# Optimization experiments

Measured on AMD Instinct MI355X. Metric: run time of the kernel, lower is better.

## Reference

```python
import jax, jax.numpy as jnp
import numpy as np

B, N = 2, 6
C_IN, C_MID = 512, 512
D, C_OUT = 112, 80
OGH, OGW, DS = 256, 704, 16
FH, FW = OGH // DS, OGW // DS  # 16, 44
D_MIN, D_MAX = 2.0, 58.0
NX, NY, NZ = 128, 128, 1
VSIZE = np.array([0.8, 0.8, 8.0], dtype=np.float32)
VCOORD = np.array([-51.2 + 0.4, -51.2 + 0.4, -5.0 + 4.0], dtype=np.float32)


def make_frustum():
    # (D, FH, FW, 4) with entries (x_pix, y_pix, depth, 1)
    ones = jnp.ones((D, FH, FW), jnp.float32)
    d = jnp.linspace(D_MIN, D_MAX, D)[:, None, None] * jnp.ones((1, FH, FW))
    x = jnp.linspace(0.0, OGW - 1.0, FW)[None, None, :] * jnp.ones((D, FH, 1))
    y = jnp.linspace(0.0, OGH - 1.0, FH)[None, :, None] * jnp.ones((D, 1, FW))
    return jnp.stack([x, y, d, ones], axis=-1)


def setup_inputs() -> dict:
    key = jax.random.key(0)
    ks = jax.random.split(key, 24)
    eye = jnp.eye(4, dtype=jnp.float32)
    K = jnp.array([[1266.0, 0.0, 800.0, 0.0],
                   [0.0, 1266.0, 450.0, 0.0],
                   [0.0, 0.0, 1.0, 0.0],
                   [0.0, 0.0, 0.0, 1.0]], jnp.float32)
    inp = {
        'feat': jax.random.normal(ks[0], (B * N, C_IN, FH, FW), jnp.float32),
        'w1': 0.05 * jax.random.normal(ks[1], (C_MID, C_IN, 3, 3), jnp.float32),
        'g1': 1.0 + 0.1 * jax.random.normal(ks[2], (C_MID,), jnp.float32),
        'b1': 0.1 * jax.random.normal(ks[3], (C_MID,), jnp.float32),
        'm1': 0.1 * jax.random.normal(ks[4], (C_MID,), jnp.float32),
        'v1': 0.5 + jax.random.uniform(ks[5], (C_MID,), jnp.float32),
        'w2': 0.05 * jax.random.normal(ks[6], (C_MID, C_MID, 3, 3), jnp.float32),
        'g2': 1.0 + 0.1 * jax.random.normal(ks[7], (C_MID,), jnp.float32),
        'b2': 0.1 * jax.random.normal(ks[8], (C_MID,), jnp.float32),
        'm2': 0.1 * jax.random.normal(ks[9], (C_MID,), jnp.float32),
        'v2': 0.5 + jax.random.uniform(ks[10], (C_MID,), jnp.float32),
        'w_out': 0.05 * jax.random.normal(ks[11], (D + C_OUT, C_MID, 1, 1), jnp.float32),
        'b_out': 0.1 * jax.random.normal(ks[12], (D + C_OUT,), jnp.float32),
        'sensor2ego': eye + 0.05 * jax.random.normal(ks[13], (B, N, 4, 4), jnp.float32),
        'sensor2virtual': eye + 0.05 * jax.random.normal(ks[14], (B, N, 4, 4), jnp.float32),
        'intrin': K + 0.01 * jax.random.normal(ks[15], (B, N, 4, 4), jnp.float32),
        'ida': eye + 0.01 * jax.random.normal(ks[16], (B, N, 4, 4), jnp.float32),
        'ref_heights': 1.5 + 0.2 * jax.random.normal(ks[17], (B, N), jnp.float32),
        'bda': eye + 0.01 * jax.random.normal(ks[18], (B, 4, 4), jnp.float32),
    }
    return inp


def _conv(x, w, p):
    return jax.lax.conv_general_dilated(x, w, (1, 1), [(p, p), (p, p)],
                                         dimension_numbers=('NCHW', 'OIHW', 'NCHW'))


def _bn(x, g, b, m, v):
    s = (g / jnp.sqrt(v + 1e-5))
    return (x - m[None, :, None, None]) * s[None, :, None, None] + b[None, :, None, None]


def get_geometry(sensor2ego, sensor2virtual, intrin, ida, ref_heights, bda):
    frustum = make_frustum()[..., None]  # (D,FH,FW,4,1)
    pts = jnp.linalg.inv(ida)[:, :, None, None, None] @ frustum  # (B,N,D,FH,FW,4,1)
    ref = ref_heights[:, :, None, None, None, None]
    height = -pts[..., 2, :] + ref  # (B,N,D,FH,FW,1)
    pc = pts.at[..., 2, :].set(10.0)
    pc = jnp.concatenate([pc[..., :2, :] * pc[..., 2:3, :], pc[..., 2:, :]], axis=-2)
    cv = sensor2virtual @ jnp.linalg.inv(intrin)
    pv = cv[:, :, None, None, None] @ pc
    ratio = height[..., 0] / pv[..., 1, 0]  # (B,N,D,FH,FW)
    pts = pv * ratio[..., None, None]
    pts = pts.at[..., 3, :].set(1.0)
    ce = sensor2ego @ jnp.linalg.inv(sensor2virtual)
    pts = ce[:, :, None, None, None] @ pts
    pts = (bda[:, None, None, None, None] @ pts)[..., 0]
    return pts[..., :3]  # (B,N,D,FH,FW,3)


def reference(feat, w1, g1, b1, m1, v1, w2, g2, b2, m2, v2, w_out, b_out,
              sensor2ego, sensor2virtual, intrin, ida, ref_heights, bda):
    # DepthNet head
    h = jax.nn.relu(_bn(_conv(feat, w1, 1), g1, b1, m1, v1))
    h = jax.nn.relu(_bn(_conv(h, w2, 1), g2, b2, m2, v2))
    hf = _conv(h, w_out, 0) + b_out[None, :, None, None]  # (B*N, D+C, FH, FW)
    depth = jax.nn.softmax(hf[:, :D], axis=1).reshape(B, N, D, FH, FW)
    context = hf[:, D:].reshape(B, N, C_OUT, FH, FW)

    geom = get_geometry(sensor2ego, sensor2virtual, intrin, ida, ref_heights, bda)

    # voxel indices
    vsize = jnp.asarray(VSIZE)
    vcoord = jnp.asarray(VCOORD)
    idx = ((geom - (vcoord - vsize / 2.0)) / vsize).astype(jnp.int32)
    valid = (jnp.all(idx >= 0, axis=-1) & (idx[..., 0] < NX)
             & (idx[..., 1] < NY) & (idx[..., 2] < NZ))

    # LSS outer product: (B,N,D,FH,FW,C)
    vol = jnp.einsum('bndhw,bnchw->bndhwc', depth, context)
    YX = NY * NX
    sid = idx[..., 1] * NX + idx[..., 0] + jnp.arange(B, dtype=jnp.int32)[:, None, None, None, None] * YX
    sid = jnp.where(valid, sid, B * YX).reshape(-1)
    bev = jax.ops.segment_sum(vol.reshape(-1, C_OUT), sid, num_segments=B * YX + 1)[:B * YX]
    return bev.reshape(B, NY, NX, C_OUT).transpose(0, 3, 1, 2)  # (B,C,NY,NX)
```

## Files before the change

### kernel.cpp

```cpp
#include <hip/hip_runtime.h>
#include <stdint.h>

#define NB   2
#define NN   6
#define NIMG 12
#define CIN  512
#define CMID 512
#define DD   112
#define COUT 80
#define FHh  16
#define FWw  44
#define NPIX 704
#define NPOS 8448
#define KK   4608
#define NXg  128
#define NYg  128
#define YX   16384
#define MAT_STRIDE 56
#define PADPIX 828
#define PROW 46
#define KSPLIT 4
#define KCHUNK (KK/KSPLIT)

typedef short short8 __attribute__((ext_vector_type(8)));
typedef float f32x4  __attribute__((ext_vector_type(4)));

#define GLD16(g, l) __builtin_amdgcn_global_load_lds((const __attribute__((address_space(1))) void*)(g), (__attribute__((address_space(3))) void*)(l), 16, 0, 0)

__device__ __forceinline__ unsigned short f2bf(float f){
  unsigned u = __float_as_uint(f);
  u += 0x7fffu + ((u >> 16) & 1u);
  return (unsigned short)(u >> 16);
}
__device__ __forceinline__ float bf2f(unsigned short u){
  return __uint_as_float(((unsigned)u) << 16);
}

__device__ __forceinline__ f32x4 mfma16(short8 a, short8 b, f32x4 c){
  return __builtin_amdgcn_mfma_f32_16x16x32_bf16(a, b, c, 0, 0, 0);
}

#define N1 (CMID*KK)
__global__ void k_prep_misc(const float* __restrict__ w1, const float* __restrict__ w2,
                            const float* __restrict__ wout,
                            const float* __restrict__ g1, const float* __restrict__ b1,
                            const float* __restrict__ m1, const float* __restrict__ v1,
                            const float* __restrict__ g2, const float* __restrict__ b2,
                            const float* __restrict__ m2, const float* __restrict__ v2,
                            unsigned short* __restrict__ wb1, unsigned short* __restrict__ wb2,
                            unsigned short* __restrict__ wb3,
                            float* __restrict__ scale1, float* __restrict__ bias1,
                            float* __restrict__ scale2, float* __restrict__ bias2){
  int i = blockIdx.x*blockDim.x + threadIdx.x;
  if (i < 2*N1){
    const float* w = (i < N1) ? w1 : w2;
    unsigned short* wb = (i < N1) ? wb1 : wb2;
    int j = (i < N1) ? i : i - N1;
    int oc = j / KK; int jj = j - oc*KK;
    int r = jj >> 9; int ic = jj & 511;
    wb[j] = f2bf(w[(size_t)(oc*512 + ic)*9 + r]);
  } else if (i < 2*N1 + 192*CMID){
    int j = i - 2*N1;
    wb3[j] = f2bf(wout[j]);
  } else if (i < 2*N1 + 192*CMID + 512){
    int t = i - (2*N1 + 192*CMID);
    float s = g1[t] / sqrtf(v1[t] + 1e-5f);
    scale1[t] = s; bias1[t] = b1[t] - m1[t]*s;
  } else if (i < 2*N1 + 192*CMID + 1024){
    int t = i - (2*N1 + 192*CMID + 512);
    float s = g2[t] / sqrtf(v2[t] + 1e-5f);
    scale2[t] = s; bias2[t] = b2[t] - m2[t]*s;
  }
}

__global__ void k_zeropad(unsigned short* __restrict__ a, unsigned short* __restrict__ b){
  int i = blockIdx.x*blockDim.x + threadIdx.x;
  int img = i >> 16; int j = i & 65535;
  int seg = j >> 9, ch = j & 511;
  int pp;
  if (seg < 46)       pp = seg;
  else if (seg < 92)  pp = 17*PROW + (seg - 46);
  else { int s2 = seg - 92; int y = s2 >> 1; pp = y*PROW + ((s2 & 1) ? 45 : 0); }
  size_t off = (size_t)img*PADPIX*512 + (size_t)pp*512 + ch;
  a[off] = 0; b[off] = 0;
}

__global__ void k_featpad(const float* __restrict__ feat, unsigned short* __restrict__ dst){
  int blk = blockIdx.x;
  int img = blk >> 4, y = blk & 15;
  const float* s = feat + (size_t)img*CIN*NPIX + y*FWw;
  unsigned short* d = dst + (size_t)img*PADPIX*512 + ((y+1)*PROW + 1)*512;
  for (int j = threadIdx.x; j < FWw*512; j += 256){
    int x = j >> 9, ic = j & 511;
    d[x*512 + ic] = f2bf(s[(size_t)ic*NPIX + x]);
  }
}

__device__ void inv4(const double* A, double* out){
  double M[4][8];
  for (int i=0;i<4;i++){ for(int j=0;j<4;j++){ M[i][j]=A[i*4+j]; M[i][4+j]=(i==j)?1.0:0.0; } }
  for (int c=0;c<4;c++){
    int piv=c; double best=fabs(M[c][c]);
    for (int r=c+1;r<4;r++){ double a=fabs(M[r][c]); if(a>best){best=a;piv=r;} }
    if (piv!=c){ for(int j=0;j<8;j++){ double tt=M[c][j]; M[c][j]=M[piv][j]; M[piv][j]=tt; } }
    double inv = 1.0 / M[c][c];
    for (int j=0;j<8;j++) M[c][j]*=inv;
    for (int r=0;r<4;r++){ if(r==c) continue; double f=M[r][c];
      for (int j=0;j<8;j++) M[r][j]-=f*M[c][j]; }
  }
  for (int i=0;i<4;i++) for(int j=0;j<4;j++) out[i*4+j]=M[i][4+j];
}
__device__ void mm4(const double* A, const double* Bm, double* C){
  for (int i=0;i<4;i++) for(int j=0;j<4;j++){
    double s=0.0; for(int k=0;k<4;k++) s+=A[i*4+k]*Bm[k*4+j]; C[i*4+j]=s; }
}

__global__ void k_prep_mats(const float* __restrict__ s2e, const float* __restrict__ s2v,
                            const float* __restrict__ intr, const float* __restrict__ ida,
                            const float* __restrict__ refh, const float* __restrict__ bda,
                            double* __restrict__ mats){
  int t = threadIdx.x;
  if (t >= NIMG) return;
  int b = t / NN;
  double Mida[16], Ms2v[16], Mintr[16], Ms2e[16], Mbda[16];
  for (int i=0;i<16;i++){
    Mida[i] =(double)ida [t*16+i];
    Ms2v[i] =(double)s2v [t*16+i];
    Mintr[i]=(double)intr[t*16+i];
    Ms2e[i] =(double)s2e [t*16+i];
    Mbda[i] =(double)bda [b*16+i];
  }
  double* o = mats + (size_t)t*MAT_STRIDE;
  double tmp[16], tmp2[16];
  inv4(Mida, o);
  inv4(Mintr, tmp);  mm4(Ms2v, tmp, o+16);
  inv4(Ms2v, tmp);   mm4(Ms2e, tmp, tmp2);
  mm4(Mbda, tmp2, o+32);
  o[48] = (double)refh[t];
}

__global__ void k_geom(const double* __restrict__ mats, int* __restrict__ sid){
  int g = blockIdx.x*blockDim.x + threadIdx.x;
  int img = g / (DD*NPIX); int rem = g - img*(DD*NPIX);
  int d = rem / NPIX; int p = rem - d*NPIX;
  int h = p / FWw; int w = p - h*FWw;
  const double* M = mats + (size_t)img*MAT_STRIDE;
  float xf = (float)w * (703.0f/43.0f);
  float yf = (float)h * 17.0f;
  float df = 2.0f + (float)d * (56.0f/111.0f);
  double x = (double)xf, y = (double)yf, dep = (double)df;
  double p0 = M[0]*x + M[1]*y + M[2]*dep + M[3];
  double p1 = M[4]*x + M[5]*y + M[6]*dep + M[7];
  double p2 = M[8]*x + M[9]*y + M[10]*dep + M[11];
  double p3 = M[12]*x + M[13]*y + M[14]*dep + M[15];
  double height = M[48] - p2;
  double c0 = p0*10.0, c1 = p1*10.0, c2 = 10.0, c3 = p3;
  const double* C = M + 16;
  double q0 = C[0]*c0 + C[1]*c1 + C[2]*c2 + C[3]*c3;
  double q1 = C[4]*c0 + C[5]*c1 + C[6]*c2 + C[7]*c3;
  double q2 = C[8]*c0 + C[9]*c1 + C[10]*c2 + C[11]*c3;
  double ratio = height / q1;
  double r0 = q0*ratio, r1 = q1*ratio, r2 = q2*ratio, r3 = 1.0;
  const double* F = M + 32;
  double gx = F[0]*r0 + F[1]*r1 + F[2]*r2 + F[3]*r3;
  double gy = F[4]*r0 + F[5]*r1 + F[6]*r2 + F[7]*r3;
  double gz = F[8]*r0 + F[9]*r1 + F[10]*r2 + F[11]*r3;
  float gxf = (float)gx, gyf = (float)gy, gzf = (float)gz;
  const float vcx = (float)(-51.2 + 0.4);
  const float ox = vcx - 0.4f;
  const float oy = ox;
  const float oz = -1.0f - 4.0f;
  float tx = (gxf - ox) / 0.8f;
  float ty = (gyf - oy) / 0.8f;
  float tz = (gzf - oz) / 8.0f;
  int ix = (int)tx, iy = (int)ty, iz = (int)tz;
  bool valid = (tx==tx) && (ty==ty) && (tz==tz) &&
               (ix >= 0) && (ix < NXg) && (iy >= 0) && (iy < NYg) && (iz == 0);
  int b = img / NN;
  sid[g] = valid ? (b*YX + iy*NXg + ix) : -1;
}

__global__ __launch_bounds__(256, 4) void k_conv_sk(const unsigned short* __restrict__ W,
    const unsigned short* __restrict__ src, unsigned short* __restrict__ part){
  __shared__ __align__(16) short As[128*32];
  __shared__ __align__(16) short Bs[128*32];
  int t = threadIdx.x;
  int lane = t & 63, wv = t >> 6;
  int wm = wv >> 1, wn = wv & 1;
  int q = lane >> 4, ml = lane & 15;
  int m0 = blockIdx.x * 128;
  int n0 = blockIdx.y * 128;
  int k0 = blockIdx.z * KCHUNK;

  int lrow = lane >> 2;
  int lcol = (lane & 3) * 8;
  const unsigned short* agp[2];
  const unsigned short* bgp[2];
  #pragma unroll
  for (int i=0;i<2;i++){
    int seg = wv*2 + i;
    agp[i] = W + (size_t)(m0 + seg*16 + lrow)*KK + lcol;
    int pos = n0 + seg*16 + lrow;
    int img = pos / NPIX; int p = pos - img*NPIX;
    int y = p / FWw; int x = p - y*FWw;
    bgp[i] = src + (size_t)img*PADPIX*512 + ((y+1)*PROW + (x+1))*512 + lcol;
  }

  f32x4 acc[4][4];
  #pragma unroll
  for (int i=0;i<4;i++)
    #pragma unroll
    for (int j=0;j<4;j++) acc[i][j] = (f32x4)0.0f;

  for (int kb = k0; kb < k0 + KCHUNK; kb += 32){
    int r = kb >> 9;
    int ic0 = kb & 511;
    int r3 = r / 3;
    int koff = (r3*PROW + (r - r3*3))*512 + ic0 - (PROW+1)*512;
    #pragma unroll
    for (int i=0;i<2;i++){
      int seg = wv*2 + i;
      GLD16(agp[i] + kb,   (char*)As + seg*1024);
      GLD16(bgp[i] + koff, (char*)Bs + seg*1024);
    }
    __syncthreads();
    short8 fa[4], fb[4];
    #pragma unroll
    for (int mi=0;mi<4;mi++) fa[mi] = *(const short8*)(As + (wm*64 + mi*16 + ml)*32 + q*8);
    #pragma unroll
    for (int ni=0;ni<4;ni++) fb[ni] = *(const short8*)(Bs + (wn*64 + ni*16 + ml)*32 + q*8);
    #pragma unroll
    for (int mi=0;mi<4;mi++)
      #pragma unroll
      for (int ni=0;ni<4;ni++)
        acc[mi][ni] = mfma16(fb[ni], fa[mi], acc[mi][ni]);
    __syncthreads();
  }

  unsigned short* op = part + (size_t)blockIdx.z*NPOS*CMID;
  #pragma unroll
  for (int mi=0;mi<4;mi++){
    int oc = m0 + wm*64 + mi*16 + ml;
    #pragma unroll
    for (int ni=0;ni<4;ni++){
      f32x4 v = acc[mi][ni];
      #pragma unroll
      for (int rr=0;rr<4;rr++){
        int pos = n0 + wn*64 + ni*16 + q*4 + rr;
        op[(size_t)pos*CMID + oc] = f2bf(v[rr]);
      }
    }
  }
}

template<int OUT_PADDED>
__global__ void k_reduce(const unsigned short* __restrict__ part,
                         const float* __restrict__ scale, const float* __restrict__ bias,
                         unsigned short* __restrict__ out){
  int i2 = blockIdx.x*blockDim.x + threadIdx.x;
  int e0 = i2*2;
  const size_t S = (size_t)NPOS*CMID;
  unsigned p0 = *(const unsigned*)(part + e0);
  unsigned p1 = *(const unsigned*)(part + e0 + S);
  unsigned p2 = *(const unsigned*)(part + e0 + 2*S);
  unsigned p3 = *(const unsigned*)(part + e0 + 3*S);
  float s0 = bf2f((unsigned short)p0) + bf2f((unsigned short)p1)
           + bf2f((unsigned short)p2) + bf2f((unsigned short)p3);
  float s1 = bf2f((unsigned short)(p0>>16)) + bf2f((unsigned short)(p1>>16))
           + bf2f((unsigned short)(p2>>16)) + bf2f((unsigned short)(p3>>16));
  int pos = e0 >> 9, oc = e0 & 511;
  float v0 = fmaxf(s0*scale[oc]   + bias[oc],   0.0f);
  float v1 = fmaxf(s1*scale[oc+1] + bias[oc+1], 0.0f);
  unsigned packed = (unsigned)f2bf(v0) | ((unsigned)f2bf(v1) << 16);
  if (OUT_PADDED){
    int img = pos / NPIX; int p = pos - img*NPIX;
    int y = p / FWw; int x = p - y*FWw;
    *(unsigned*)(out + (size_t)img*PADPIX*512 + ((y+1)*PROW + (x+1))*512 + oc) = packed;
  } else {
    *(unsigned*)(out + e0) = packed;
  }
}

__global__ __launch_bounds__(256) void k_gemm64(const unsigned short* __restrict__ A,
    const unsigned short* __restrict__ Bt, const float* __restrict__ bout,
    float* __restrict__ hf){
  const int K = 512;
  __shared__ __align__(16) short As[64][32];
  __shared__ __align__(16) short Bs[128][32];
  int t = threadIdx.x;
  int m0 = blockIdx.x*64; int n0 = blockIdx.y*128;
  int lane = t & 63; int wv = t >> 6; int q = lane >> 4, ml = lane & 15;
  f32x4 acc[8];
  #pragma unroll
  for (int i=0;i<8;i++) acc[i] = (f32x4)0.0f;
  int ar = t >> 2, ac = (t & 3) * 8;
  int br = t >> 1, bc = (t & 1) * 16;
  const unsigned short* pa = A  + (size_t)(m0 + ar)*K + ac;
  const unsigned short* pb = Bt + (size_t)(n0 + br)*K + bc;
  for (int kb = 0; kb < K; kb += 32){
    uint4 av = *(const uint4*)(pa + kb);
    uint4 b0 = *(const uint4*)(pb + kb);
    uint4 b1 = *(const uint4*)(pb + kb + 8);
    __syncthreads();
    *(uint4*)&As[ar][ac] = av;
    *(uint4*)&Bs[br][bc] = b0; *(uint4*)&Bs[br][bc+8] = b1;
    __syncthreads();
    short8 fa = *(const short8*)&As[wv*16 + ml][q*8];
    #pragma unroll
    for (int ni=0;ni<8;ni++){
      short8 fb = *(const short8*)&Bs[ni*16 + ml][q*8];
      acc[ni] = mfma16(fb, fa, acc[ni]);
    }
  }
  int oc = m0 + wv*16 + ml;
  float bb = bout[oc];
  #pragma unroll
  for (int ni=0;ni<8;ni++)
    #pragma unroll
    for (int r=0;r<4;r++){
      int pos = n0 + ni*16 + q*4 + r;
      hf[(size_t)pos*192 + oc] = acc[ni][r] + bb;
    }
}

__global__ void k_softmax(const float* __restrict__ hf, float* __restrict__ depth){
  int pos = blockIdx.x*4 + (threadIdx.x >> 6);
  int lane = threadIdx.x & 63;
  const float* row = hf + (size_t)pos*192;
  float v0 = row[lane];
  float v1 = (lane < DD-64) ? row[64 + lane] : -1e30f;
  float mx = fmaxf(v0, v1);
  #pragma unroll
  for (int m=1; m<64; m<<=1) mx = fmaxf(mx, __shfl_xor(mx, m, 64));
  float e0 = expf(v0 - mx);
  float e1 = (lane < DD-64) ? expf(v1 - mx) : 0.0f;
  float s = e0 + e1;
  #pragma unroll
  for (int m=1; m<64; m<<=1) s += __shfl_xor(s, m, 64);
  float inv = 1.0f / s;
  depth[(size_t)pos*DD + lane] = e0 * inv;
  if (lane < DD-64) depth[(size_t)pos*DD + 64 + lane] = e1 * inv;
}

__global__ void k_scatter(const float* __restrict__ depth, const float* __restrict__ hf,
                          const int* __restrict__ sidb, float* __restrict__ bev){
  int pos = blockIdx.x;
  int img = pos / NPIX; int p = pos - img*NPIX;
  __shared__ float sdep[DD];
  __shared__ int   ssid[DD];
  __shared__ float sctx[COUT];
  __shared__ float cwt[DD];
  __shared__ int   cvox[DD];
  __shared__ int   scnt;
  int t = threadIdx.x;
  if (t == 0) scnt = 0;
  if (t < DD){
    sdep[t] = depth[(size_t)pos*DD + t];
    ssid[t] = sidb[(size_t)(img*DD + t)*NPIX + p];
  }
  if (t < COUT) sctx[t] = hf[(size_t)pos*192 + DD + t];
  __syncthreads();
  if (t < DD){
    int s = ssid[t];
    bool head = (s >= 0) && (t == 0 || ssid[t-1] != s);
    if (head){
      float w = 0.0f;
      for (int dd = t; dd < DD && ssid[dd] == s; ++dd) w += sdep[dd];
      int i = atomicAdd(&scnt, 1);
      cvox[i] = s; cwt[i] = w;
    }
  }
  __syncthreads();
  int H = scnt;
  for (int j = t; j < H*COUT; j += 128){
    int h = j / COUT, c = j - h*COUT;
    atomicAdd(&bev[(size_t)cvox[h]*COUT + c], cwt[h]*sctx[c]);
  }
}

__global__ __launch_bounds__(256) void k_transpose(const float* __restrict__ bev, float* __restrict__ out){
  __shared__ float tile[64*COUT];
  int blk = blockIdx.x;
  int b = blk >> 8; int yx0 = (blk & 255) * 64;
  int t = threadIdx.x;
  const float* src = bev + ((size_t)b*YX + yx0)*COUT;
  for (int j = t; j < 64*COUT; j += 256) tile[j] = src[j];
  __syncthreads();
  float* dst = out + (size_t)b*COUT*YX + yx0;
  for (int j = t; j < COUT*64; j += 256){
    int c = j >> 6, row = j & 63;
    dst[(size_t)c*YX + row] = tile[row*COUT + c];
  }
}

extern "C" void kernel_launch(void* const* d_in, const int* in_sizes, int n_in,
                              void* d_out, int out_size, void* d_ws, size_t ws_size,
                              hipStream_t stream) {
  const float* feat = (const float*)d_in[0];
  const float* w1   = (const float*)d_in[1];
  const float* g1   = (const float*)d_in[2];
  const float* b1   = (const float*)d_in[3];
  const float* m1   = (const float*)d_in[4];
  const float* v1   = (const float*)d_in[5];
  const float* w2   = (const float*)d_in[6];
  const float* g2   = (const float*)d_in[7];
  const float* b2   = (const float*)d_in[8];
  const float* m2   = (const float*)d_in[9];
  const float* v2   = (const float*)d_in[10];
  const float* wout = (const float*)d_in[11];
  const float* bout = (const float*)d_in[12];
  const float* s2e  = (const float*)d_in[13];
  const float* s2v  = (const float*)d_in[14];
  const float* intr = (const float*)d_in[15];
  const float* ida  = (const float*)d_in[16];
  const float* refh = (const float*)d_in[17];
  const float* bda  = (const float*)d_in[18];

  uint8_t* base = (uint8_t*)d_ws;
  size_t off = 0;
  auto alloc = [&](size_t bytes)->void*{
    void* r = base + off;
    off = (off + bytes + 255) & ~(size_t)255;
    return r;
  };
  unsigned short* wb1 = (unsigned short*)alloc((size_t)CMID*KK*2);
  unsigned short* wb2 = (unsigned short*)alloc((size_t)CMID*KK*2);
  unsigned short* wb3 = (unsigned short*)alloc((size_t)192*CMID*2);
  float* scale1 = (float*)alloc(CMID*4);
  float* bias1  = (float*)alloc(CMID*4);
  float* scale2 = (float*)alloc(CMID*4);
  float* bias2  = (float*)alloc(CMID*4);
  double* mats  = (double*)alloc((size_t)NIMG*MAT_STRIDE*8);

  size_t padded_bytes = (size_t)NIMG*PADPIX*512*2;
  uint8_t* regionE = (uint8_t*)alloc(padded_bytes);
  uint8_t* regionF = (uint8_t*)alloc(padded_bytes);
  float* depth = (float*)alloc((size_t)NPOS*DD*4);
  int*   sid   = (int*)  alloc((size_t)NIMG*DD*NPIX*4);
  float* bev   = (float*)alloc((size_t)NB*YX*COUT*4);
  unsigned short* part = (unsigned short*)alloc((size_t)KSPLIT*NPOS*CMID*2);

  unsigned short* featpad = (unsigned short*)regionE;
  unsigned short* h2      = (unsigned short*)regionE;
  unsigned short* h1pad   = (unsigned short*)regionF;
  float*          hf      = (float*)regionF;

  int prep_n = 2*N1 + 192*CMID + 1024;
  k_prep_misc<<<(prep_n + 255)/256, 256, 0, stream>>>(w1, w2, wout, g1, b1, m1, v1,
      g2, b2, m2, v2, wb1, wb2, wb3, scale1, bias1, scale2, bias2);
  k_prep_mats<<<1, 64, 0, stream>>>(s2e, s2v, intr, ida, refh, bda, mats);
  k_geom<<<3696, 256, 0, stream>>>(mats, sid);

  k_zeropad<<<3072, 256, 0, stream>>>(featpad, h1pad);
  k_featpad<<<192, 256, 0, stream>>>(feat, featpad);

  k_conv_sk<<<dim3(4, 66, KSPLIT), 256, 0, stream>>>(wb1, featpad, part);
  k_reduce<1><<<NPOS*CMID/512, 256, 0, stream>>>(part, scale1, bias1, h1pad);
  k_conv_sk<<<dim3(4, 66, KSPLIT), 256, 0, stream>>>(wb2, h1pad, part);
  k_reduce<0><<<NPOS*CMID/512, 256, 0, stream>>>(part, scale2, bias2, h2);
  k_gemm64<<<dim3(3, 66), 256, 0, stream>>>(wb3, h2, bout, hf);

  k_softmax<<<2112, 256, 0, stream>>>(hf, depth);

  hipMemsetAsync(bev, 0, (size_t)NB*YX*COUT*4, stream);
  k_scatter<<<NPOS, 128, 0, stream>>>(depth, hf, sid, bev);

  k_transpose<<<512, 256, 0, stream>>>(bev, (float*)d_out);
}
```

Before: 394.8 us.

## Double-buffer conv LDS loads, remap blocks for XCD locality, transpose featpad via LDS

The split-K conv kernel now double-buffers its A/B LDS tiles. It issues the next stage's global-to-LDS loads before computing the current one and uses explicit waitcnt and barriers, so memory latency overlaps with the MFMAs. Blocks are launched on a 1D grid with a swizzled mapping, so that consecutive chiplet-assigned blocks share the same N/K tile and get better cache reuse. The feature pad/convert kernel now transposes through a shared-memory tile so that reads are coalesced and writes are packed pairs. The BEV memset is folded into the zero-pad kernel to remove one launch. The double buffering doubles LDS use, which may lower occupancy under launch_bounds(256,4).

```diff
diff --git a/kernel.cpp b/kernel.cpp
--- a/kernel.cpp
+++ b/kernel.cpp
@@ -21,6 +21,7 @@
 #define PROW 46
 #define KSPLIT 4
 #define KCHUNK (KK/KSPLIT)
+#define NSTEP (KCHUNK/32)
 
 typedef short short8 __attribute__((ext_vector_type(8)));
 typedef float f32x4  __attribute__((ext_vector_type(4)));
@@ -73,8 +74,10 @@
   }
 }
 
-__global__ void k_zeropad(unsigned short* __restrict__ a, unsigned short* __restrict__ b){
+__global__ void k_zeropad(unsigned short* __restrict__ a, unsigned short* __restrict__ b,
+                          float4* __restrict__ bev){
   int i = blockIdx.x*blockDim.x + threadIdx.x;
+  if (i < NB*YX*COUT/4) bev[i] = make_float4(0.f,0.f,0.f,0.f);
   int img = i >> 16; int j = i & 65535;
   int seg = j >> 9, ch = j & 511;
   int pp;
@@ -85,14 +88,24 @@
   a[off] = 0; b[off] = 0;
 }
 
-__global__ void k_featpad(const float* __restrict__ feat, unsigned short* __restrict__ dst){
+__global__ __launch_bounds__(256) void k_featpad(const float* __restrict__ feat,
+                                                 unsigned short* __restrict__ dst){
+  __shared__ float tile[32][65];
   int blk = blockIdx.x;
-  int img = blk >> 4, y = blk & 15;
-  const float* s = feat + (size_t)img*CIN*NPIX + y*FWw;
-  unsigned short* d = dst + (size_t)img*PADPIX*512 + ((y+1)*PROW + 1)*512;
-  for (int j = threadIdx.x; j < FWw*512; j += 256){
-    int x = j >> 9, ic = j & 511;
-    d[x*512 + ic] = f2bf(s[(size_t)ic*NPIX + x]);
+  int img = blk / 176; int r = blk - img*176;
+  int cb = r / 11; int pb = r - cb*11;
+  int c0 = cb*32, p0 = pb*64;
+  int t = threadIdx.x;
+  const float* s = feat + (size_t)img*CIN*NPIX + (size_t)c0*NPIX + p0;
+  for (int ch = t>>6; ch < 32; ch += 4)
+    tile[ch][t & 63] = s[(size_t)ch*NPIX + (t & 63)];
+  __syncthreads();
+  int ch = (t & 15)*2;
+  for (int pix = t>>4; pix < 64; pix += 16){
+    int p = p0 + pix;
+    int y = p / FWw, x = p - y*FWw;
+    unsigned v = (unsigned)f2bf(tile[ch][pix]) | ((unsigned)f2bf(tile[ch+1][pix]) << 16);
+    *(unsigned*)(dst + (size_t)img*PADPIX*512 + ((y+1)*PROW + (x+1))*512 + c0 + ch) = v;
   }
 }
 
@@ -182,15 +195,19 @@
 
 __global__ __launch_bounds__(256, 4) void k_conv_sk(const unsigned short* __restrict__ W,
     const unsigned short* __restrict__ src, unsigned short* __restrict__ part){
-  __shared__ __align__(16) short As[128*32];
-  __shared__ __align__(16) short Bs[128*32];
+  __shared__ __align__(16) short As[2][128*32];
+  __shared__ __align__(16) short Bs[2][128*32];
   int t = threadIdx.x;
   int lane = t & 63, wv = t >> 6;
   int wm = wv >> 1, wn = wv & 1;
   int q = lane >> 4, ml = lane & 15;
-  int m0 = blockIdx.x * 128;
-  int n0 = blockIdx.y * 128;
-  int k0 = blockIdx.z * KCHUNK;
+
+  int id = blockIdx.x;
+  int res = id & 7, slot = id >> 3;
+  int g = res + 8*(slot >> 2);
+  int mblk = slot & 3;
+  int z = g / 66, n = g - z*66;
+  int m0 = mblk*128, n0 = n*128, k0 = z*KCHUNK;
 
   int lrow = lane >> 2;
   int lcol = (lane & 3) * 8;
@@ -212,7 +229,9 @@
     #pragma unroll
     for (int j=0;j<4;j++) acc[i][j] = (f32x4)0.0f;
 
-  for (int kb = k0; kb < k0 + KCHUNK; kb += 32){
+  auto stage = [&](int step){
+    int kb = k0 + step*32;
+    int d = step & 1;
     int r = kb >> 9;
     int ic0 = kb & 511;
     int r3 = r / 3;
@@ -220,24 +239,36 @@
     #pragma unroll
     for (int i=0;i<2;i++){
       int seg = wv*2 + i;
-      GLD16(agp[i] + kb,   (char*)As + seg*1024);
-      GLD16(bgp[i] + koff, (char*)Bs + seg*1024);
-    }
-    __syncthreads();
+      GLD16(agp[i] + kb,   (char*)As[d] + seg*1024);
+      GLD16(bgp[i] + koff, (char*)Bs[d] + seg*1024);
+    }
+  };
+
+  stage(0);
+  for (int k = 0; k < NSTEP; ++k){
+    if (k + 1 < NSTEP){
+      stage(k + 1);
+      asm volatile("s_waitcnt vmcnt(4)" ::: "memory");
+    } else {
+      asm volatile("s_waitcnt vmcnt(0)" ::: "memory");
+    }
+    asm volatile("s_barrier" ::: "memory");
+    const short* Ab = As[k & 1];
+    const short* Bb = Bs[k & 1];
     short8 fa[4], fb[4];
     #pragma unroll
-    for (int mi=0;mi<4;mi++) fa[mi] = *(const short8*)(As + (wm*64 + mi*16 + ml)*32 + q*8);
-    #pragma unroll
-    for (int ni=0;ni<4;ni++) fb[ni] = *(const short8*)(Bs + (wn*64 + ni*16 + ml)*32 + q*8);
+    for (int mi=0;mi<4;mi++) fa[mi] = *(const short8*)(Ab + (wm*64 + mi*16 + ml)*32 + q*8);
+    #pragma unroll
+    for (int ni=0;ni<4;ni++) fb[ni] = *(const short8*)(Bb + (wn*64 + ni*16 + ml)*32 + q*8);
     #pragma unroll
     for (int mi=0;mi<4;mi++)
       #pragma unroll
       for (int ni=0;ni<4;ni++)
         acc[mi][ni] = mfma16(fb[ni], fa[mi], acc[mi][ni]);
-    __syncthreads();
-  }
-
-  unsigned short* op = part + (size_t)blockIdx.z*NPOS*CMID;
+    asm volatile("s_barrier" ::: "memory");
+  }
+
+  unsigned short* op = part + (size_t)z*NPOS*CMID;
   #pragma unroll
   for (int mi=0;mi<4;mi++){
     int oc = m0 + wm*64 + mi*16 + ml;
@@ -451,18 +482,17 @@
   k_prep_mats<<<1, 64, 0, stream>>>(s2e, s2v, intr, ida, refh, bda, mats);
   k_geom<<<3696, 256, 0, stream>>>(mats, sid);
 
-  k_zeropad<<<3072, 256, 0, stream>>>(featpad, h1pad);
-  k_featpad<<<192, 256, 0, stream>>>(feat, featpad);
-
-  k_conv_sk<<<dim3(4, 66, KSPLIT), 256, 0, stream>>>(wb1, featpad, part);
+  k_zeropad<<<3072, 256, 0, stream>>>(featpad, h1pad, (float4*)bev);
+  k_featpad<<<2112, 256, 0, stream>>>(feat, featpad);
+
+  k_conv_sk<<<1056, 256, 0, stream>>>(wb1, featpad, part);
   k_reduce<1><<<NPOS*CMID/512, 256, 0, stream>>>(part, scale1, bias1, h1pad);
-  k_conv_sk<<<dim3(4, 66, KSPLIT), 256, 0, stream>>>(wb2, h1pad, part);
+  k_conv_sk<<<1056, 256, 0, stream>>>(wb2, h1pad, part);
   k_reduce<0><<<NPOS*CMID/512, 256, 0, stream>>>(part, scale2, bias2, h2);
   k_gemm64<<<dim3(3, 66), 256, 0, stream>>>(wb3, h2, bout, hf);
 
   k_softmax<<<2112, 256, 0, stream>>>(hf, depth);
 
-  hipMemsetAsync(bev, 0, (size_t)NB*YX*COUT*4, stream);
   k_scatter<<<NPOS, 128, 0, stream>>>(depth, hf, sid, bev);
 
   k_transpose<<<512, 256, 0, stream>>>(bev, (float*)d_out);
```

New measurement: 371.1 us. -6.0%, faster.
